# Optimization experiments

Hardware: AMD Instinct MI355X
Metric: run time of the kernel (lower is better)

Reference implementation:

```python
import jax, jax.numpy as jnp
import numpy as np

N_G, E_G = 76800, 307200   # gg: line graph over bonds
N_L, E_L = 38400, 153600   # lg: atom graph; E_L == 2*N_G
B = 64                     # number of molecules (equal-sized subgraphs)
H = 8                      # attention heads
BOND, ATOM, IN_E, FE1 = 40, 92, 10, 36


def _egat_layer(nfeats, efeats, src, dst, N, W_node, b_node, W_ni, W_nj, W_fij, attn, bias, Fn, Fe):
    # edge scores: gather + add (u_add_v) + edge proj + bias, leaky_relu
    f_edge = (nfeats @ W_ni)[src] + (nfeats @ W_nj)[dst] + efeats @ W_fij + bias
    f_out = jax.nn.leaky_relu(f_edge).reshape(-1, H, Fe)         # [E,H,Fe]
    e = jnp.einsum('ehf,hf->eh', f_out, attn)                     # [E,H]
    # edge softmax over incoming edges of each destination node
    m = jax.lax.stop_gradient(jax.ops.segment_max(e, dst, num_segments=N))
    ex = jnp.exp(e - m[dst])
    a = ex / jax.ops.segment_sum(ex, dst, num_segments=N)[dst]    # [E,H]
    h = (nfeats @ W_node + b_node).reshape(-1, H, Fn)             # [N,H,Fn]
    h_out = jax.ops.segment_sum(h[src] * a[:, :, None], dst, num_segments=N)
    return h_out, f_out


def setup_inputs() -> dict:
    key = jax.random.key(0)
    ks = iter(jax.random.split(key, 64))
    def lin(i, o):
        return jax.random.normal(next(ks), (i, o), jnp.float32) * (1.0 / np.sqrt(i))
    inp = {}
    inp['gg_src'] = jax.random.randint(next(ks), (E_G,), 0, N_G, jnp.int32)
    inp['gg_dst'] = jnp.concatenate([jnp.arange(N_G, dtype=jnp.int32),
                                     jax.random.randint(next(ks), (E_G - N_G,), 0, N_G, jnp.int32)])
    inp['gg_nfeat'] = jax.random.normal(next(ks), (N_G, BOND), jnp.float32)
    inp['gg_efeat'] = jax.random.normal(next(ks), (E_G, IN_E), jnp.float32)
    inp['lg_src'] = jax.random.randint(next(ks), (E_L,), 0, N_L, jnp.int32)
    inp['lg_dst'] = jnp.concatenate([jnp.arange(N_L, dtype=jnp.int32),
                                     jax.random.randint(next(ks), (E_L - N_L,), 0, N_L, jnp.int32)])
    inp['lg_nfeat'] = jax.random.normal(next(ks), (N_L, ATOM), jnp.float32)
    inp['lg_efeat'] = jax.random.normal(next(ks), (E_L, BOND), jnp.float32)
    # layer1 (on gg): in_node=BOND, in_edge=IN_E, out_node=BOND, out_edge=FE1
    inp['W_node1'] = lin(BOND, H * BOND); inp['b_node1'] = jnp.zeros((H * BOND,), jnp.float32)
    inp['W_ni1'] = lin(BOND, H * FE1); inp['W_nj1'] = lin(BOND, H * FE1)
    inp['W_fij1'] = lin(IN_E, H * FE1)
    inp['attn1'] = jax.random.normal(next(ks), (H, FE1), jnp.float32) * 0.1
    inp['bias1'] = jnp.zeros((H * FE1,), jnp.float32)
    # layers 2a/2b (on lg): in_node=ATOM, in_edge=BOND, out_node=ATOM, out_edge=BOND
    for sfx in ('2a', '2b'):
        inp['W_node' + sfx] = lin(ATOM, H * ATOM); inp['b_node' + sfx] = jnp.zeros((H * ATOM,), jnp.float32)
        inp['W_ni' + sfx] = lin(ATOM, H * BOND); inp['W_nj' + sfx] = lin(ATOM, H * BOND)
        inp['W_fij' + sfx] = lin(BOND, H * BOND)
        inp['attn' + sfx] = jax.random.normal(next(ks), (H, BOND), jnp.float32) * 0.1
        inp['bias' + sfx] = jnp.zeros((H * BOND,), jnp.float32)
    # Readout: Linear(128,128) + Sigmoid + Linear(128,1) + Sigmoid
    inp['Wr1'] = lin(ATOM + FE1, 128); inp['br1'] = jnp.zeros((128,), jnp.float32)
    inp['Wr2'] = lin(128, 1); inp['br2'] = jnp.zeros((1,), jnp.float32)
    return inp


def reference(gg_src, gg_dst, gg_nfeat, gg_efeat, lg_src, lg_dst, lg_nfeat, lg_efeat,
              W_node1, b_node1, W_ni1, W_nj1, W_fij1, attn1, bias1,
              W_node2a, b_node2a, W_ni2a, W_nj2a, W_fij2a, attn2a, bias2a,
              W_node2b, b_node2b, W_ni2b, W_nj2b, W_fij2b, attn2b, bias2b,
              Wr1, br1, Wr2, br2):
    # stage 1: EGAT on gg, then sum over heads
    n1, e1 = _egat_layer(gg_nfeat, gg_efeat, gg_src, gg_dst, N_G,
                         W_node1, b_node1, W_ni1, W_nj1, W_fij1, attn1, bias1, BOND, FE1)
    y2n = n1.sum(axis=1)       # [N_G, BOND]
    y22 = e1.sum(axis=1)       # [E_G, FE1]
    # each gg-node feature repeated twice, added to lg edge features
    ef = jnp.repeat(y2n, 2, axis=0) + lg_efeat   # [E_L, BOND]
    nf = lg_nfeat
    nf, e2 = _egat_layer(nf, ef, lg_src, lg_dst, N_L,
                         W_node2a, b_node2a, W_ni2a, W_nj2a, W_fij2a, attn2a, bias2a, ATOM, BOND)
    nf = nf.sum(axis=1); ef = e2.sum(axis=1)
    nf, e2 = _egat_layer(nf, ef, lg_src, lg_dst, N_L,
                         W_node2b, b_node2b, W_ni2b, W_nj2b, W_fij2b, attn2b, bias2b, ATOM, BOND)
    nf = nf.sum(axis=1)
    # per-subgraph average pooling (equal-size subgraphs -> reshape mean).
    # NOTE: original pool_subgraphs(y_22, gg) slices an edge-indexed tensor by node
    # counts (upstream quirk); reproduced exactly by taking the first N_G rows.
    y1 = nf.reshape(B, N_L // B, ATOM).mean(axis=1)          # [B, ATOM]
    y2 = y22[:N_G].reshape(B, N_G // B, FE1).mean(axis=1)    # [B, FE1]
    y = jnp.concatenate([y1, y2], axis=1)                     # [B, 128]
    h = jax.nn.sigmoid(y @ Wr1 + br1)
    return jax.nn.sigmoid(h @ Wr2 + br2)                      # [B, 1]
```

## Files before the change

kernel.cpp:

```cpp
#include <hip/hip_runtime.h>
#include <math.h>

#define NG 76800
#define EG 307200
#define NL 38400
#define EL 153600
#define NB 64
#define NH 8

typedef __attribute__((ext_vector_type(8))) short bf16x8;
typedef __attribute__((ext_vector_type(4))) float f32x4;
typedef unsigned short u16;

__device__ __forceinline__ float sigmoidf(float x) { return 1.f / (1.f + expf(-x)); }
__device__ __forceinline__ u16 f2bf(float x) {
    unsigned u = __float_as_uint(x);
    return (u16)((u + 0x7FFFu + ((u >> 16) & 1u)) >> 16);
}
__device__ __forceinline__ float bf2f(u16 v) { return __uint_as_float(((unsigned)v) << 16); }

__global__ __launch_bounds__(256) void convert_pad_kernel(const float* __restrict__ src,
                                                          u16* __restrict__ dst,
                                                          int M, int K, int Kpad) {
    int i = blockIdx.x * 256 + threadIdx.x;
    if (i >= M * Kpad) return;
    int m = i / Kpad, k = i - m * Kpad;
    dst[i] = (k < K) ? f2bf(src[(size_t)m * K + k]) : (u16)0;
}

__global__ __launch_bounds__(256) void wtrans_kernel(const float* __restrict__ W, int ldw,
                                                     u16* __restrict__ dst,
                                                     int K, int N, int Nalloc, int Kpad) {
    int i = blockIdx.x * 256 + threadIdx.x;
    if (i >= Nalloc * Kpad) return;
    int n = i / Kpad, k = i - n * Kpad;
    dst[i] = (n < N && k < K) ? f2bf(W[(size_t)k * ldw + n]) : (u16)0;
}

__global__ __launch_bounds__(256) void wtrans_hp_kernel(const float* __restrict__ W, int ldw,
                                                        u16* __restrict__ dst,
                                                        int K, int Kpad) {
    int i = blockIdx.x * 256 + threadIdx.x;
    if (i >= 320 * Kpad) return;
    int n = i / Kpad, k = i - n * Kpad;
    int hh = n / 40, f = n - hh * 40;
    float v = (k < K && f < 36) ? W[(size_t)k * ldw + hh * 36 + f] : 0.f;
    dst[i] = f2bf(v);
}

__global__ __launch_bounds__(256) void meta_kernel(const float* __restrict__ attn1,
                                                   const float* __restrict__ bias1,
                                                   const float* __restrict__ b2a,
                                                   const float* __restrict__ b2b,
                                                   float* __restrict__ attn_p1,
                                                   float* __restrict__ bias_cat1,
                                                   float* __restrict__ bias_cat2a,
                                                   float* __restrict__ bias_cat2b) {
    int i = blockIdx.x * 256 + threadIdx.x;
    if (i < 320) {
        int hh = i / 40, f = i - hh * 40;
        attn_p1[i] = (f < 36) ? attn1[hh * 36 + f] : 0.f;
    } else if (i < 960) {
        int j = i - 320;
        float v = 0.f;
        if (j < 320) {
            int hh = j / 40, f = j - hh * 40;
            v = (f < 36) ? bias1[hh * 36 + f] : 0.f;
        }
        bias_cat1[j] = v;
    } else if (i < 1600) {
        int j = i - 960;
        bias_cat2a[j] = (j < 320) ? b2a[j] : 0.f;
    } else if (i < 2240) {
        int j = i - 1600;
        bias_cat2b[j] = (j < 320) ? b2b[j] : 0.f;
    }
}

template <int KPAD>
__global__ __launch_bounds__(256) void gemm_bf_kernel(const u16* __restrict__ A,
                                                      const u16* __restrict__ Wt,
                                                      const float* __restrict__ bias,
                                                      u16* __restrict__ C, int Ncols,
                                                      int Nstride) {
    __shared__ u16 st[4][16 * 72];
    const int m0 = blockIdx.x * 64;
    const int n0 = blockIdx.y * 64;
    const int wv = threadIdx.x >> 6;
    const int lane = threadIdx.x & 63;
    const int q = lane >> 4;
    const int mr = lane & 15;

    const u16* Arow = A + (size_t)(m0 + wv * 16 + mr) * KPAD;
    f32x4 acc[4];
#pragma unroll
    for (int t = 0; t < 4; ++t) acc[t] = (f32x4){0.f, 0.f, 0.f, 0.f};

#pragma unroll
    for (int k0 = 0; k0 < KPAD; k0 += 32) {
        bf16x8 af = *(const bf16x8*)(Arow + k0 + q * 8);
#pragma unroll
        for (int t = 0; t < 4; ++t) {
            bf16x8 bv = *(const bf16x8*)(Wt + (size_t)(n0 + t * 16 + mr) * KPAD + k0 + q * 8);
            acc[t] = __builtin_amdgcn_mfma_f32_16x16x32_bf16(af, bv, acc[t], 0, 0, 0);
        }
    }

    u16* myst = st[wv];
#pragma unroll
    for (int t = 0; t < 4; ++t) {
        const int colme = n0 + t * 16 + mr;
        const float bb = (bias && colme < Ncols) ? bias[colme] : 0.f;
#pragma unroll
        for (int r = 0; r < 4; ++r)
            myst[(q * 4 + r) * 72 + t * 16 + mr] = f2bf(acc[t][r]);
    }
    const int rrow = lane >> 3;
    const int rcol = (lane & 7) * 8;
    bf16x8 v0 = *(const bf16x8*)(myst + rrow * 72 + rcol);
    bf16x8 v1 = *(const bf16x8*)(myst + (rrow + 8) * 72 + rcol);
    const int gcol = n0 + rcol;
    if (gcol < Ncols) {
        const int grow = m0 + wv * 16 + rrow;
        *(bf16x8*)(C + (size_t)grow * Nstride + gcol) = v0;
        *(bf16x8*)(C + (size_t)(grow + 8) * Nstride + gcol) = v1;
    }
}

__global__ __launch_bounds__(256) void ef2a_kernel(const float* __restrict__ lg_ef,
                                                   const float* __restrict__ y2n,
                                                   u16* __restrict__ dst) {
    int i = blockIdx.x * 256 + threadIdx.x;
    if (i >= EL * 64) return;
    int e = i >> 6, c = i & 63;
    dst[i] = (c < 40) ? f2bf(lg_ef[(size_t)e * 40 + c] + y2n[(size_t)(e >> 1) * 40 + c]) : (u16)0;
}

template <int KPAD, int FSMODE>
__global__ __launch_bounds__(512) void pe_edge_kernel(
    const u16* __restrict__ A,
    const u16* __restrict__ Wt,
    const int* __restrict__ src, const int* __restrict__ dst,
    const u16* __restrict__ Pn,
    const float* __restrict__ attn,
    float* __restrict__ esc,
    void* __restrict__ fsum,
    int e0, int CH, int fsumE) {
    __shared__ u16 pe[64][328];
    const int wv = threadIdx.x >> 6;
    const int lane = threadIdx.x & 63;
    const int q = lane >> 4;
    const int mr = lane & 15;
    const int m0 = blockIdx.x * 64;

    {
        const int rg0 = (wv & 3) * 16;
        const int t0 = (wv >> 2) * 10;
        const u16* Arow = A + (size_t)(m0 + rg0 + mr) * KPAD;
        f32x4 acc[10];
#pragma unroll
        for (int t = 0; t < 10; ++t) acc[t] = (f32x4){0.f, 0.f, 0.f, 0.f};
#pragma unroll
        for (int k0 = 0; k0 < KPAD; k0 += 32) {
            bf16x8 af = *(const bf16x8*)(Arow + k0 + q * 8);
#pragma unroll
            for (int t = 0; t < 10; ++t) {
                bf16x8 bv = *(const bf16x8*)(Wt + (size_t)((t0 + t) * 16 + mr) * KPAD + k0 + q * 8);
                acc[t] = __builtin_amdgcn_mfma_f32_16x16x32_bf16(af, bv, acc[t], 0, 0, 0);
            }
        }
#pragma unroll
        for (int t = 0; t < 10; ++t)
#pragma unroll
            for (int r = 0; r < 4; ++r)
                pe[rg0 + q * 4 + r][(t0 + t) * 16 + mr] = f2bf(acc[t][r]);
    }
    __syncthreads();

    const int lc = (lane < 40) ? lane : 39;
    const int h = lc / 5, o = lc - h * 5;
    const int c = h * 40 + o * 8;
    const bool act = (lane < 40);

    float attn_r[8];
#pragma unroll
    for (int j = 0; j < 8; ++j) attn_r[j] = attn[c + j];

    for (int ei = 0; ei < 8; ++ei) {
        const int row = wv * 8 + ei;
        const int e = e0 + m0 + row;
        const int s = src[e], d = dst[e];
        bf16x8 api = *(const bf16x8*)(Pn + (size_t)s * 640 + c);
        bf16x8 apj = *(const bf16x8*)(Pn + (size_t)d * 640 + 320 + c);
        bf16x8 ape = *(const bf16x8*)(&pe[row][c]);

        float v[8];
        float ehp = 0.f;
#pragma unroll
        for (int j = 0; j < 8; ++j) {
            float x = bf2f((u16)api[j]) + bf2f((u16)apj[j]) + bf2f((u16)ape[j]);
            x = x > 0.f ? x : 0.01f * x;
            v[j] = x;
            ehp += x * attn_r[j];
        }
        float eh = 0.f;
#pragma unroll
        for (int k = 0; k < 5; ++k) eh += __shfl(ehp, h * 5 + k, 64);
        if (act && o == 0) esc[(size_t)e * 8 + h] = eh;

        if (FSMODE != 0 && e < fsumE) {
#pragma unroll
            for (int m = 4; m >= 1; m >>= 1) {
                const int p = (h ^ m) * 5 + o;
#pragma unroll
                for (int j = 0; j < 8; ++j) v[j] += __shfl(v[j], p, 64);
            }
            if (act && h == 0) {
#pragma unroll
                for (int j = 0; j < 8; ++j) {
                    const int f = o * 8 + j;
                    if (FSMODE == 1) {
                        if (f < 36) ((float*)fsum)[(size_t)e * 36 + f] = v[j];
                    } else {
                        ((u16*)fsum)[(size_t)e * 64 + f] = f2bf(v[j]);
                    }
                }
            }
        }
    }
}

__global__ __launch_bounds__(256) void hist_kernel(const int* __restrict__ dst,
                                                   int* __restrict__ cnt, int E) {
    int i = blockIdx.x * 256 + threadIdx.x;
    if (i < E) atomicAdd(&cnt[dst[i]], 1);
}

__global__ __launch_bounds__(1024) void scan_block_kernel(const int* __restrict__ cnt,
                                                          int* __restrict__ excl,
                                                          int* __restrict__ bsum, int N) {
    __shared__ int sd[1024];
    const int tid = threadIdx.x;
    const int i = blockIdx.x * 1024 + tid;
    int v = (i < N) ? cnt[i] : 0;
    sd[tid] = v;
    __syncthreads();
    for (int off = 1; off < 1024; off <<= 1) {
        int t = (tid >= off) ? sd[tid - off] : 0;
        __syncthreads();
        sd[tid] += t;
        __syncthreads();
    }
    if (i < N) excl[i] = sd[tid] - v;
    if (tid == 1023) bsum[blockIdx.x] = sd[1023];
}

__global__ void scan_top_kernel(int* __restrict__ bsum, int nblk) {
    if (threadIdx.x == 0 && blockIdx.x == 0) {
        int run = 0;
        for (int b = 0; b < nblk; ++b) {
            int t = bsum[b];
            bsum[b] = run;
            run += t;
        }
    }
}

__global__ __launch_bounds__(256) void scan_add_kernel(int* __restrict__ row_ptr,
                                                       const int* __restrict__ bsum,
                                                       int N, int E) {
    int i = blockIdx.x * 256 + threadIdx.x;
    if (i < N) row_ptr[i] += bsum[i >> 10];
    if (i == 0) row_ptr[N] = E;
}

__global__ __launch_bounds__(256) void scatter_kernel(const int* __restrict__ dst,
                                                      const int* __restrict__ src,
                                                      const int* __restrict__ row_ptr,
                                                      int* __restrict__ cur,
                                                      int* __restrict__ eidx,
                                                      int* __restrict__ srcs, int E) {
    int i = blockIdx.x * 256 + threadIdx.x;
    if (i < E) {
        int d = dst[i];
        int pos = row_ptr[d] + atomicAdd(&cur[d], 1);
        eidx[pos] = i;
        srcs[pos] = src[i];
    }
}

template <int GH>
__global__ __launch_bounds__(256) void csr_softmax_kernel(
    const int* __restrict__ row_ptr, const int* __restrict__ eidx,
    const float* __restrict__ esc, float* __restrict__ wcsr, int N) {
    constexpr int NS = 64 / GH;
    const int wid = threadIdx.x >> 6;
    const int lane = threadIdx.x & 63;
    const int nid = blockIdx.x * 4 + wid;
    if (nid >= N) return;
    const int r0 = row_ptr[nid], r1 = row_ptr[nid + 1];
    const int h = lane & (GH - 1);
    const int slot = lane / GH;

    float mx = -1e30f;
    for (int i = r0 + slot; i < r1; i += NS)
        mx = fmaxf(mx, esc[(size_t)eidx[i] * GH + h]);
#pragma unroll
    for (int m = GH; m < 64; m <<= 1) mx = fmaxf(mx, __shfl_xor(mx, m, 64));

    float den = 0.f;
    for (int i = r0 + slot; i < r1; i += NS)
        den += expf(esc[(size_t)eidx[i] * GH + h] - mx);
#pragma unroll
    for (int m = GH; m < 64; m <<= 1) den += __shfl_xor(den, m, 64);
    const float rden = 1.f / den;

    for (int i = r0 + slot; i < r1; i += NS)
        wcsr[(size_t)i * GH + h] = expf(esc[(size_t)eidx[i] * GH + h] - mx) * rden;
}

template <int Fn, int GH, int OM, int STR>
__global__ __launch_bounds__(256) void node_agg_kernel(
    const int* __restrict__ row_ptr,
    const int* __restrict__ srcs,
    const float* __restrict__ wcsr,
    const u16* __restrict__ Pnode,
    void* __restrict__ outp, int N) {
    constexpr int PAIRS = Fn / 2;
    const int wid = threadIdx.x >> 6;
    const int lane = threadIdx.x & 63;
    const int nid = blockIdx.x * 4 + wid;
    if (nid >= N) return;
    const int r0 = row_ptr[nid], r1 = row_ptr[nid + 1];
    const int col = 2 * lane;
    const bool act = (lane < PAIRS);

    float a0 = 0.f, a1 = 0.f;
    for (int i = r0; i < r1; i += 4) {
        const u16* prs[4];
        float wv[4][GH];
#pragma unroll
        for (int b = 0; b < 4; ++b) {
            const int ii = (i + b < r1) ? (i + b) : (r1 - 1);
            prs[b] = Pnode + (size_t)srcs[ii] * STR;
            const float live = (i + b < r1) ? 1.f : 0.f;
            const float* wp = wcsr + (size_t)ii * GH;
#pragma unroll
            for (int hh = 0; hh < GH; ++hh) wv[b][hh] = wp[hh] * live;
        }
        if (act) {
            unsigned pv[4][GH];
#pragma unroll
            for (int b = 0; b < 4; ++b)
#pragma unroll
                for (int hh = 0; hh < GH; ++hh)
                    pv[b][hh] = *(const unsigned*)(prs[b] + hh * Fn + col);
#pragma unroll
            for (int b = 0; b < 4; ++b)
#pragma unroll
                for (int hh = 0; hh < GH; ++hh) {
                    a0 += wv[b][hh] * bf2f((u16)(pv[b][hh] & 0xFFFFu));
                    a1 += wv[b][hh] * bf2f((u16)(pv[b][hh] >> 16));
                }
        }
    }
    if (OM == 0) {
        if (act) {
            float* op = (float*)outp + (size_t)nid * Fn + col;
            op[0] = a0;
            op[1] = a1;
        }
    } else {
        unsigned* ob = (unsigned*)((u16*)outp + (size_t)nid * 96);
        if (act) {
            unsigned pk = (unsigned)f2bf(a0) | ((unsigned)f2bf(a1) << 16);
            ob[lane] = pk;
        } else if (lane < 48) {
            ob[lane] = 0u;
        }
    }
}

__global__ __launch_bounds__(256) void readout_kernel(const u16* __restrict__ nfb,
                                                      const float* __restrict__ y22p,
                                                      const float* __restrict__ Wr1,
                                                      const float* __restrict__ br1,
                                                      const float* __restrict__ Wr2,
                                                      const float* __restrict__ br2,
                                                      float* __restrict__ out) {
    const int b = blockIdx.x;
    const int t = threadIdx.x;
    __shared__ float y[128];
    __shared__ float hh[128];
    __shared__ float red[128];
    if (t < 92) {
        float s = 0.f;
        const u16* base = nfb + (size_t)b * 600 * 96 + t;
        for (int i = 0; i < 600; ++i) s += bf2f(base[(size_t)i * 96]);
        y[t] = s * (1.f / 600.f);
    } else if (t >= 128 && t < 164) {
        int f = t - 128;
        float s = 0.f;
        const float* base = y22p + (size_t)b * 1200 * 36 + f;
        for (int i = 0; i < 1200; ++i) s += base[(size_t)i * 36];
        y[92 + f] = s * (1.f / 1200.f);
    }
    __syncthreads();
    if (t < 128) {
        float s = br1[t];
        for (int c = 0; c < 128; ++c) s += y[c] * Wr1[(size_t)c * 128 + t];
        hh[t] = sigmoidf(s);
    }
    __syncthreads();
    if (t < 128) red[t] = hh[t] * Wr2[t];
    __syncthreads();
    for (int k = 64; k > 0; k >>= 1) {
        if (t < k) red[t] += red[t + k];
        __syncthreads();
    }
    if (t == 0) out[b] = sigmoidf(red[0] + br2[0]);
}

static inline int cdiv(int a, int b) { return (a + b - 1) / b; }

extern "C" void kernel_launch(void* const* d_in, const int* in_sizes, int n_in,
                              void* d_out, int out_size, void* d_ws, size_t ws_size,
                              hipStream_t stream) {
    const int* gg_src = (const int*)d_in[0];
    const int* gg_dst = (const int*)d_in[1];
    const float* gg_nf = (const float*)d_in[2];
    const float* gg_ef = (const float*)d_in[3];
    const int* lg_src = (const int*)d_in[4];
    const int* lg_dst = (const int*)d_in[5];
    const float* lg_nf = (const float*)d_in[6];
    const float* lg_ef = (const float*)d_in[7];
    const float* W_node1 = (const float*)d_in[8];
    const float* b_node1 = (const float*)d_in[9];
    const float* W_ni1 = (const float*)d_in[10];
    const float* W_nj1 = (const float*)d_in[11];
    const float* W_fij1 = (const float*)d_in[12];
    const float* attn1 = (const float*)d_in[13];
    const float* bias1 = (const float*)d_in[14];
    const float* W_node2a = (const float*)d_in[15];
    const float* b_node2a = (const float*)d_in[16];
    const float* W_ni2a = (const float*)d_in[17];
    const float* W_nj2a = (const float*)d_in[18];
    const float* W_fij2a = (const float*)d_in[19];
    const float* attn2a = (const float*)d_in[20];
    const float* bias2a = (const float*)d_in[21];
    const float* W_node2b = (const float*)d_in[22];
    const float* b_node2b = (const float*)d_in[23];
    const float* W_ni2b = (const float*)d_in[24];
    const float* W_nj2b = (const float*)d_in[25];
    const float* W_fij2b = (const float*)d_in[26];
    const float* attn2b = (const float*)d_in[27];
    const float* bias2b = (const float*)d_in[28];
    const float* Wr1 = (const float*)d_in[29];
    const float* br1 = (const float*)d_in[30];
    const float* Wr2 = (const float*)d_in[31];
    const float* br2 = (const float*)d_in[32];
    float* out = (float*)d_out;

    char* ws = (char*)d_ws;
    size_t off = 0;
    auto take = [&](size_t bytes) {
        size_t o = off;
        off += (bytes + 255) & ~(size_t)255;
        return (void*)(ws + o);
    };
    float* y2n = (float*)take((size_t)NG * 40 * 4);
    float* y22p = (float*)take((size_t)NG * 36 * 4);
    float* esc = (float*)take((size_t)EG * 8 * 4);
    float* wcsr = (float*)take((size_t)EG * 8 * 4);
    int* gg_row = (int*)take((size_t)(NG + 1) * 4);
    int* gg_eidx = (int*)take((size_t)EG * 4);
    int* gg_srcs = (int*)take((size_t)EG * 4);
    int* gg_cnt = (int*)take((size_t)NG * 4);
    int* lg_row = (int*)take((size_t)(NL + 1) * 4);
    int* lg_eidx = (int*)take((size_t)EL * 4);
    int* lg_srcs = (int*)take((size_t)EL * 4);
    int* lg_cnt = (int*)take((size_t)NL * 4);
    int* bsum = (int*)take((size_t)128 * 4);
    u16* gg_nf_bf = (u16*)take((size_t)NG * 64 * 2);
    u16* gg_ef_bf = (u16*)take((size_t)EG * 32 * 2);
    u16* lg_nf_bf = (u16*)take((size_t)NL * 96 * 2);
    u16* nfa_bf = (u16*)take((size_t)NL * 96 * 2);
    u16* nfb_bf = (u16*)take((size_t)NL * 96 * 2);
    u16* ef_shared = (u16*)take((size_t)EL * 64 * 2);
    u16* wt_ninj1 = (u16*)take((size_t)640 * 64 * 2);
    u16* wt_node1 = (u16*)take((size_t)320 * 64 * 2);
    u16* wt_fij1 = (u16*)take((size_t)320 * 32 * 2);
    u16* wt_ninj2a = (u16*)take((size_t)640 * 96 * 2);
    u16* wt_ninj2b = (u16*)take((size_t)640 * 96 * 2);
    u16* wt_fij2a = (u16*)take((size_t)320 * 64 * 2);
    u16* wt_fij2b = (u16*)take((size_t)320 * 64 * 2);
    u16* wt_node2a = (u16*)take((size_t)768 * 96 * 2);
    u16* wt_node2b = (u16*)take((size_t)768 * 96 * 2);
    float* attn_p1 = (float*)take((size_t)320 * 4);
    float* bias_cat1 = (float*)take((size_t)640 * 4);
    float* bias_cat2a = (float*)take((size_t)640 * 4);
    float* bias_cat2b = (float*)take((size_t)640 * 4);
    u16* slab = (u16*)take(((size_t)NG * 640 + (size_t)(EG / 4) * 320) * 2);

    auto cvt = [&](const float* s, u16* d, int M, int K, int Kpad) {
        convert_pad_kernel<<<cdiv(M * Kpad, 256), 256, 0, stream>>>(s, d, M, K, Kpad);
    };
    auto wtr = [&](const float* W, int ldw, u16* d, int K, int N, int Nalloc, int Kpad) {
        wtrans_kernel<<<cdiv(Nalloc * Kpad, 256), 256, 0, stream>>>(W, ldw, d, K, N, Nalloc, Kpad);
    };
    auto build_csr = [&](const int* dst, const int* src, int* row_ptr, int* eidx, int* srcs,
                         int* cnt, int N, int E) {
        hipMemsetAsync(cnt, 0, (size_t)N * 4, stream);
        hist_kernel<<<cdiv(E, 256), 256, 0, stream>>>(dst, cnt, E);
        int nblk = cdiv(N, 1024);
        scan_block_kernel<<<nblk, 1024, 0, stream>>>(cnt, row_ptr, bsum, N);
        scan_top_kernel<<<1, 64, 0, stream>>>(bsum, nblk);
        scan_add_kernel<<<cdiv(N, 256), 256, 0, stream>>>(row_ptr, bsum, N, E);
        hipMemsetAsync(cnt, 0, (size_t)N * 4, stream);
        scatter_kernel<<<cdiv(E, 256), 256, 0, stream>>>(dst, src, row_ptr, cnt, eidx, srcs, E);
    };

    build_csr(gg_dst, gg_src, gg_row, gg_eidx, gg_srcs, gg_cnt, NG, EG);
    build_csr(lg_dst, lg_src, lg_row, lg_eidx, lg_srcs, lg_cnt, NL, EL);

    cvt(gg_nf, gg_nf_bf, NG, 40, 64);
    cvt(gg_ef, gg_ef_bf, EG, 10, 32);
    cvt(lg_nf, lg_nf_bf, NL, 92, 96);
    wtrans_hp_kernel<<<cdiv(320 * 64, 256), 256, 0, stream>>>(W_ni1, 288, wt_ninj1, 40, 64);
    wtrans_hp_kernel<<<cdiv(320 * 64, 256), 256, 0, stream>>>(W_nj1, 288, wt_ninj1 + 320 * 64, 40, 64);
    wtrans_hp_kernel<<<cdiv(320 * 32, 256), 256, 0, stream>>>(W_fij1, 288, wt_fij1, 10, 32);
    wtr(W_node1, 320, wt_node1, 40, 320, 320, 64);
    wtr(W_ni2a, 320, wt_ninj2a, 92, 320, 320, 96);
    wtr(W_nj2a, 320, wt_ninj2a + 320 * 96, 92, 320, 320, 96);
    wtr(W_ni2b, 320, wt_ninj2b, 92, 320, 320, 96);
    wtr(W_nj2b, 320, wt_ninj2b + 320 * 96, 92, 320, 320, 96);
    wtr(W_fij2a, 320, wt_fij2a, 40, 320, 320, 64);
    wtr(W_fij2b, 320, wt_fij2b, 40, 320, 320, 64);
    wtr(W_node2a, 736, wt_node2a, 92, 736, 768, 96);
    wtr(W_node2b, 736, wt_node2b, 92, 736, 768, 96);
    meta_kernel<<<cdiv(2240, 256), 256, 0, stream>>>(attn1, bias1, bias2a, bias2b,
                                                     attn_p1, bias_cat1, bias_cat2a, bias_cat2b);

    {
        u16* Pn1 = slab;
        gemm_bf_kernel<64><<<dim3(NG / 64, 10), 256, 0, stream>>>(
            gg_nf_bf, wt_ninj1, bias_cat1, Pn1, 640, 640);
        for (int ch = 0; ch < 4; ++ch) {
            const int e0 = ch * (EG / 4);
            pe_edge_kernel<32, 1><<<(EG / 4) / 64, 512, 0, stream>>>(
                gg_ef_bf + (size_t)e0 * 32, wt_fij1, gg_src, gg_dst, Pn1,
                attn_p1, esc, y22p, e0, EG / 4, NG);
        }
        csr_softmax_kernel<8><<<NG / 4, 256, 0, stream>>>(gg_row, gg_eidx, esc, wcsr, NG);
        u16* Pnode1 = slab;
        gemm_bf_kernel<64><<<dim3(NG / 64, 5), 256, 0, stream>>>(
            gg_nf_bf, wt_node1, b_node1, Pnode1, 320, 320);
        node_agg_kernel<40, 8, 0, 320><<<NG / 4, 256, 0, stream>>>(gg_row, gg_srcs, wcsr,
                                                                   Pnode1, y2n, NG);
    }

    ef2a_kernel<<<cdiv(EL * 64, 256), 256, 0, stream>>>(lg_ef, y2n, ef_shared);

    for (int layer = 0; layer < 2; ++layer) {
        const bool a = (layer == 0);
        const u16* nf_in = a ? lg_nf_bf : nfa_bf;
        const u16* Wninj = a ? wt_ninj2a : wt_ninj2b;
        const u16* Wfij = a ? wt_fij2a : wt_fij2b;
        const u16* Wnode = a ? wt_node2a : wt_node2b;
        const float* bn = a ? b_node2a : b_node2b;
        const float* bcat = a ? bias_cat2a : bias_cat2b;
        const float* at = a ? attn2a : attn2b;
        u16* nf_out = a ? nfa_bf : nfb_bf;

        u16* Pn2 = slab;
        gemm_bf_kernel<96><<<dim3(NL / 64, 10), 256, 0, stream>>>(nf_in, Wninj, bcat, Pn2, 640, 640);
        if (a)
            pe_edge_kernel<64, 2><<<EL / 64, 512, 0, stream>>>(
                ef_shared, Wfij, lg_src, lg_dst, Pn2, at, esc, ef_shared, 0, EL, EL);
        else
            pe_edge_kernel<64, 0><<<EL / 64, 512, 0, stream>>>(
                ef_shared, Wfij, lg_src, lg_dst, Pn2, at, esc, nullptr, 0, EL, 0);
        csr_softmax_kernel<8><<<NL / 4, 256, 0, stream>>>(lg_row, lg_eidx, esc, wcsr, NL);
        u16* Pnode2 = slab;
        gemm_bf_kernel<96><<<dim3(NL / 64, 12), 256, 0, stream>>>(nf_in, Wnode, bn, Pnode2, 736, 768);
        node_agg_kernel<92, 8, 1, 768><<<NL / 4, 256, 0, stream>>>(lg_row, lg_srcs, wcsr,
                                                                   Pnode2, nf_out, NL);
    }

    readout_kernel<<<NB, 256, 0, stream>>>(nfb_bf, y22p, Wr1, br1, Wr2, br2, out);
}
```

Baseline: 1.015 ms.

## Prefetch edge gathers, halve pe_edge block size, merge chunked launches

```diff
diff --git a/kernel.cpp b/kernel.cpp
--- a/kernel.cpp
+++ b/kernel.cpp
@@ -113,7 +113,7 @@
         const float bb = (bias && colme < Ncols) ? bias[colme] : 0.f;
 #pragma unroll
         for (int r = 0; r < 4; ++r)
-            myst[(q * 4 + r) * 72 + t * 16 + mr] = f2bf(acc[t][r]);
+            myst[(q * 4 + r) * 72 + t * 16 + mr] = f2bf(acc[t][r] + bb);
     }
     const int rrow = lane >> 3;
     const int rcol = (lane & 7) * 8;
@@ -137,7 +137,7 @@
 }
 
 template <int KPAD, int FSMODE>
-__global__ __launch_bounds__(512) void pe_edge_kernel(
+__global__ __launch_bounds__(256) void pe_edge_kernel(
     const u16* __restrict__ A,
     const u16* __restrict__ Wt,
     const int* __restrict__ src, const int* __restrict__ dst,
@@ -146,16 +146,16 @@
     float* __restrict__ esc,
     void* __restrict__ fsum,
     int e0, int CH, int fsumE) {
-    __shared__ u16 pe[64][328];
+    __shared__ u16 pe[32][328];
     const int wv = threadIdx.x >> 6;
     const int lane = threadIdx.x & 63;
     const int q = lane >> 4;
     const int mr = lane & 15;
-    const int m0 = blockIdx.x * 64;
+    const int m0 = blockIdx.x * 32;
 
     {
-        const int rg0 = (wv & 3) * 16;
-        const int t0 = (wv >> 2) * 10;
+        const int rg0 = (wv & 1) * 16;
+        const int t0 = (wv >> 1) * 10;
         const u16* Arow = A + (size_t)(m0 + rg0 + mr) * KPAD;
         f32x4 acc[10];
 #pragma unroll
@@ -186,12 +186,22 @@
 #pragma unroll
     for (int j = 0; j < 8; ++j) attn_r[j] = attn[c + j];
 
+    const int row0 = wv * 8;
+    int e = e0 + m0 + row0;
+    int s = src[e], d = dst[e];
+    bf16x8 api = *(const bf16x8*)(Pn + (size_t)s * 640 + c);
+    bf16x8 apj = *(const bf16x8*)(Pn + (size_t)d * 640 + 320 + c);
+
+#pragma unroll
     for (int ei = 0; ei < 8; ++ei) {
-        const int row = wv * 8 + ei;
-        const int e = e0 + m0 + row;
-        const int s = src[e], d = dst[e];
-        bf16x8 api = *(const bf16x8*)(Pn + (size_t)s * 640 + c);
-        bf16x8 apj = *(const bf16x8*)(Pn + (size_t)d * 640 + 320 + c);
+        bf16x8 napi, napj;
+        if (ei < 7) {
+            const int ne = e + 1;
+            const int ns = src[ne], nd = dst[ne];
+            napi = *(const bf16x8*)(Pn + (size_t)ns * 640 + c);
+            napj = *(const bf16x8*)(Pn + (size_t)nd * 640 + 320 + c);
+        }
+        const int row = row0 + ei;
         bf16x8 ape = *(const bf16x8*)(&pe[row][c]);
 
         float v[8];
@@ -227,6 +237,11 @@
                 }
             }
         }
+        if (ei < 7) {
+            api = napi;
+            apj = napj;
+        }
+        ++e;
     }
 }
 
@@ -500,7 +515,7 @@
     float* bias_cat1 = (float*)take((size_t)640 * 4);
     float* bias_cat2a = (float*)take((size_t)640 * 4);
     float* bias_cat2b = (float*)take((size_t)640 * 4);
-    u16* slab = (u16*)take(((size_t)NG * 640 + (size_t)(EG / 4) * 320) * 2);
+    u16* slab = (u16*)take((size_t)NG * 640 * 2);
 
     auto cvt = [&](const float* s, u16* d, int M, int K, int Kpad) {
         convert_pad_kernel<<<cdiv(M * Kpad, 256), 256, 0, stream>>>(s, d, M, K, Kpad);
@@ -545,12 +560,8 @@
         u16* Pn1 = slab;
         gemm_bf_kernel<64><<<dim3(NG / 64, 10), 256, 0, stream>>>(
             gg_nf_bf, wt_ninj1, bias_cat1, Pn1, 640, 640);
-        for (int ch = 0; ch < 4; ++ch) {
-            const int e0 = ch * (EG / 4);
-            pe_edge_kernel<32, 1><<<(EG / 4) / 64, 512, 0, stream>>>(
-                gg_ef_bf + (size_t)e0 * 32, wt_fij1, gg_src, gg_dst, Pn1,
-                attn_p1, esc, y22p, e0, EG / 4, NG);
-        }
+        pe_edge_kernel<32, 1><<<EG / 32, 256, 0, stream>>>(
+            gg_ef_bf, wt_fij1, gg_src, gg_dst, Pn1, attn_p1, esc, y22p, 0, EG, NG);
         csr_softmax_kernel<8><<<NG / 4, 256, 0, stream>>>(gg_row, gg_eidx, esc, wcsr, NG);
         u16* Pnode1 = slab;
         gemm_bf_kernel<64><<<dim3(NG / 64, 5), 256, 0, stream>>>(
@@ -575,10 +586,10 @@
         u16* Pn2 = slab;
         gemm_bf_kernel<96><<<dim3(NL / 64, 10), 256, 0, stream>>>(nf_in, Wninj, bcat, Pn2, 640, 640);
         if (a)
-            pe_edge_kernel<64, 2><<<EL / 64, 512, 0, stream>>>(
+            pe_edge_kernel<64, 2><<<EL / 32, 256, 0, stream>>>(
                 ef_shared, Wfij, lg_src, lg_dst, Pn2, at, esc, ef_shared, 0, EL, EL);
         else
-            pe_edge_kernel<64, 0><<<EL / 64, 512, 0, stream>>>(
+            pe_edge_kernel<64, 0><<<EL / 32, 256, 0, stream>>>(
                 ef_shared, Wfij, lg_src, lg_dst, Pn2, at, esc, nullptr, 0, EL, 0);
         csr_softmax_kernel<8><<<NL / 4, 256, 0, stream>>>(lg_row, lg_eidx, esc, wcsr, NL);
         u16* Pnode2 = slab;
```

Result: faster. 980.5 us (-3.4%).
